# Kernel optimization log

Hardware: AMD Instinct MI355X
Metric: run time of the kernel (lower is better)

Reference implementation:

```python
import jax, jax.numpy as jnp
import numpy as np

BUCKET_SIZE = 64  # init kwarg bucket_size
DIM = 64          # init kwarg dim (per-head dim, used for scaling)


def setup_inputs() -> dict:
    key = jax.random.key(0)
    kq, kk = jax.random.split(key)
    q = jax.random.normal(kq, (32, 8192, 64), dtype=jnp.float32)
    k = jax.random.normal(kk, (32, 8192, 64), dtype=jnp.float32)
    return {"q": q, "k": k}


def _cumavg(t):
    # cumulative average along the sequence axis (axis=1)
    r = jnp.arange(1, t.shape[1] + 1, dtype=t.dtype)
    return jnp.cumsum(t, axis=1) / r[None, :, None]


def reference(q, k):
    bh, n, d = q.shape
    buckets = n // BUCKET_SIZE
    kv_buckets = k.shape[1] // BUCKET_SIZE

    # bucket the cumulative averages: [bh, buckets, bucket_size, d]
    q_r = _cumavg(q).reshape(bh, buckets, BUCKET_SIZE, d)
    k_r = _cumavg(k).reshape(bh, kv_buckets, BUCKET_SIZE, d)

    sq = q_r[:, :, 0]                                   # [bh, buckets, d]
    sk = k_r.sum(axis=2)                                # [bh, kv_buckets, d]
    sk = jnp.pad(sk, ((0, 0), (1, 0), (0, 0)))          # pad one zero bucket row at front

    R = jnp.einsum('bie,bje->bij', sq, sk) * (DIM ** -0.5)  # [bh, buckets, kv_buckets+1]

    rows = jnp.arange(buckets)[:, None]
    cols = jnp.arange(kv_buckets + 1)[None, :]
    neg = -jnp.finfo(R.dtype).max
    # masked_fill: for row i, columns i+1..buckets set to -max (cols > rows)
    R = jnp.where(cols > rows, neg, R)
    R = jax.nn.softmax(R, axis=-1)
    # tril(diagonal=-1): keep entries with col < row
    R = jnp.where(cols < rows, R, jnp.zeros((), R.dtype))
    return R
```

## Files before the change

kernel.cpp:

```cpp
#include <hip/hip_runtime.h>
#include <cstddef>
#include <cstdint>

constexpr int BH = 32;
constexpr int N  = 8192;
constexpr int D  = 64;
constexpr int BK = 64;
constexpr int NB = 128;
constexpr int NC = 129;

#define GLOBAL_AS(p) ((const __attribute__((address_space(1))) uint32_t*)(p))
#define LDS_AS(p)    ((__attribute__((address_space(3))) uint32_t*)(p))

__global__ __launch_bounds__(256) void kA(const float* __restrict__ q,
                                          const float* __restrict__ k,
                                          float* __restrict__ qsum,
                                          float* __restrict__ ksum,
                                          float* __restrict__ kw,
                                          float* __restrict__ qfirst,
                                          float* __restrict__ W) {
  const int j = blockIdx.x, b = blockIdx.y;
  const int tid  = threadIdx.x;
  const int f    = tid & 15;
  const int rr   = tid >> 4;
  const int w    = tid >> 6;
  const int lane = tid & 63;
  const int base = j * BK;
  const size_t ob = ((size_t)b * NB + j) * D;

  __shared__ float4 buf4[2048];
  __shared__ float red[3][4][D];

  const float4* q4 = (const float4*)(q + ((size_t)b * N + base) * D);
  const float4* k4 = (const float4*)(k + ((size_t)b * N + base) * D);

#pragma unroll
  for (int p = 0; p < 4; ++p) {
    const int u = w * 256 + p * 64 + lane;
    __builtin_amdgcn_global_load_lds(GLOBAL_AS(q4 + u), LDS_AS(buf4 + u), 16, 0, 0);
    __builtin_amdgcn_global_load_lds(GLOBAL_AS(k4 + u), LDS_AS(buf4 + 1024 + u), 16, 0, 0);
  }

  float x = 1.0f / (float)(base + lane + 1);
#pragma unroll
  for (int s = 1; s < 64; s <<= 1) {
    const float y = __shfl_down(x, s, 64);
    if (lane + s < 64) x += y;
  }
  float tw[4];
#pragma unroll
  for (int p = 0; p < 4; ++p) tw[p] = __shfl(x, 16 * p + rr, 64);

  __syncthreads();

  float aq[4] = {0, 0, 0, 0}, ak[4] = {0, 0, 0, 0}, aw[4] = {0, 0, 0, 0};
#pragma unroll
  for (int p = 0; p < 4; ++p) {
    const float4 vq = buf4[(16 * p + rr) * 16 + f];
    const float4 vk = buf4[1024 + (16 * p + rr) * 16 + f];
    aq[0] += vq.x; aq[1] += vq.y; aq[2] += vq.z; aq[3] += vq.w;
    ak[0] += vk.x; ak[1] += vk.y; ak[2] += vk.z; ak[3] += vk.w;
    aw[0] += vk.x * tw[p]; aw[1] += vk.y * tw[p];
    aw[2] += vk.z * tw[p]; aw[3] += vk.w * tw[p];
  }

#pragma unroll
  for (int c = 0; c < 4; ++c) {
    aq[c] += __shfl_xor(aq[c], 16, 64); aq[c] += __shfl_xor(aq[c], 32, 64);
    ak[c] += __shfl_xor(ak[c], 16, 64); ak[c] += __shfl_xor(ak[c], 32, 64);
    aw[c] += __shfl_xor(aw[c], 16, 64); aw[c] += __shfl_xor(aw[c], 32, 64);
  }
  if (lane < 16) {
    ((float4*)&red[0][w][0])[f] = make_float4(aq[0], aq[1], aq[2], aq[3]);
    ((float4*)&red[1][w][0])[f] = make_float4(ak[0], ak[1], ak[2], ak[3]);
    ((float4*)&red[2][w][0])[f] = make_float4(aw[0], aw[1], aw[2], aw[3]);
  }
  if (tid < 16) {
    ((float4*)(qfirst + ob))[tid] = buf4[tid];
  }
  if (tid == 0 && b == 0) W[j] = x;
  __syncthreads();

  if (tid < 192) {
    const int arr = tid >> 6, d = tid & 63;
    const float s = red[arr][0][d] + red[arr][1][d] + red[arr][2][d] + red[arr][3][d];
    float* dst = (arr == 0) ? qsum : (arr == 1) ? ksum : kw;
    dst[ob + d] = s;
  }
}

__global__ __launch_bounds__(256) void kB(const float* __restrict__ qsum,
                                          const float* __restrict__ ksum,
                                          const float* __restrict__ kw,
                                          const float* __restrict__ qfirst,
                                          const float* __restrict__ W,
                                          float* __restrict__ sq,
                                          float* __restrict__ skp) {
  const int side = blockIdx.x;
  const int b    = blockIdx.y;
  const int tid  = threadIdx.x;
  const int d    = tid & 63;
  const int jg   = tid >> 6;

  __shared__ float buf[NB * D];
  __shared__ float tot[4 * D];
  __shared__ float Wl[NB];

  const float* src = (side == 0 ? qsum : ksum) + (size_t)b * NB * D;
  {
    const float4* g4 = (const float4*)src;
    float4* l4 = (float4*)buf;
    for (int u = tid; u < NB * D / 4; u += 256) l4[u] = g4[u];
    if (side == 1 && tid < NB) Wl[tid] = W[tid];
  }
  __syncthreads();

  float t0 = 0.0f;
  for (int jj = 0; jj < 32; ++jj) t0 += buf[(jg * 32 + jj) * D + d];
  tot[jg * D + d] = t0;
  __syncthreads();

  float pre = 0.0f;
  for (int g = 0; g < jg; ++g) pre += tot[g * D + d];

  if (side == 0) {
    for (int jj = 0; jj < 32; ++jj) {
      const int j = jg * 32 + jj;
      const size_t o = ((size_t)b * NB + j) * D + d;
      sq[o] = (pre + qfirst[o]) / (float)(j * BK + 1);
      pre += buf[j * D + d];
    }
  } else {
    if (tid < D) skp[(size_t)b * NC * D + tid] = 0.0f;
    for (int jj = 0; jj < 32; ++jj) {
      const int j = jg * 32 + jj;
      const size_t o = ((size_t)b * NB + j) * D + d;
      skp[((size_t)b * NC + j + 1) * D + d] = pre * Wl[j] + kw[o];
      pre += buf[j * D + d];
    }
  }
}

__global__ __launch_bounds__(256) void kC(const float* __restrict__ sq,
                                          const float* __restrict__ skp,
                                          float* __restrict__ out) {
  const int tile = blockIdx.x, b = blockIdx.y;
  const int tid = threadIdx.x;
  const int jp = tid & 63, rep = tid >> 6;
  const int T0 = tile * 8;
  const int rows = T0 + 8;

  __shared__ float skpS[NB * D];
  __shared__ float sqs[8 * D];

  {
    const float4* g4 = (const float4*)(skp + (size_t)b * NC * D);
    for (int u = tid; u < rows * 16; u += 256) {
      const int row = u >> 4, f = u & 15;
      ((float4*)skpS)[row * 16 + ((f + row) & 15)] = g4[u];
    }
    if (tid < 128)
      ((float4*)sqs)[tid] = ((const float4*)(sq + ((size_t)b * NB + T0) * D))[tid];
  }
  __syncthreads();

  float acc0[2] = {0, 0}, acc1[2] = {0, 0};
  const float4* sk4 = (const float4*)skpS;
  const float4* sq4 = (const float4*)sqs;
#pragma unroll
  for (int d4 = 0; d4 < 16; ++d4) {
    const int slot = (d4 + jp) & 15;
    const float4 k0 = sk4[jp * 16 + slot];
    const float4 k1 = sk4[(jp + 64) * 16 + slot];
#pragma unroll
    for (int ii = 0; ii < 2; ++ii) {
      const float4 s = sq4[(rep * 2 + ii) * 16 + d4];
      acc0[ii] += s.x * k0.x + s.y * k0.y + s.z * k0.z + s.w * k0.w;
      acc1[ii] += s.x * k1.x + s.y * k1.y + s.z * k1.z + s.w * k1.w;
    }
  }

#pragma unroll
  for (int ii = 0; ii < 2; ++ii) {
    const int i = T0 + rep * 2 + ii;
    const int j0 = jp, j1 = jp + 64;
    const float v0 = acc0[ii] * 0.125f, v1 = acc1[ii] * 0.125f;
    const bool val0 = (j0 <= i), val1 = (j1 <= i);
    float m = fmaxf(val0 ? v0 : -3.402823466e38f, val1 ? v1 : -3.402823466e38f);
#pragma unroll
    for (int s = 1; s < 64; s <<= 1) m = fmaxf(m, __shfl_xor(m, s, 64));
    const float e0 = val0 ? __expf(v0 - m) : 0.0f;
    const float e1 = val1 ? __expf(v1 - m) : 0.0f;
    float ss = e0 + e1;
#pragma unroll
    for (int s = 1; s < 64; s <<= 1) ss += __shfl_xor(ss, s, 64);
    const float rden = 1.0f / ss;
    float* orow = out + ((size_t)b * NB + i) * NC;
    orow[j0] = (j0 < i) ? e0 * rden : 0.0f;
    orow[j1] = (j1 < i) ? e1 * rden : 0.0f;
    if (jp == 0) orow[128] = 0.0f;
  }
}

extern "C" void kernel_launch(void* const* d_in, const int* in_sizes, int n_in,
                              void* d_out, int out_size, void* d_ws, size_t ws_size,
                              hipStream_t stream) {
  const float* q = (const float*)d_in[0];
  const float* k = (const float*)d_in[1];
  float* out = (float*)d_out;

  float* ws     = (float*)d_ws;
  float* qsum   = ws;
  float* ksum   = qsum   + (size_t)BH * NB * D;
  float* kw     = ksum   + (size_t)BH * NB * D;
  float* qfirst = kw     + (size_t)BH * NB * D;
  float* sq     = qfirst + (size_t)BH * NB * D;
  float* skp    = sq     + (size_t)BH * NB * D;
  float* W      = skp    + (size_t)BH * NC * D;

  kA<<<dim3(NB, BH), 256, 0, stream>>>(q, k, qsum, ksum, kw, qfirst, W);
  kB<<<dim3(2, BH), 256, 0, stream>>>(qsum, ksum, kw, qfirst, W, sq, skp);
  kC<<<dim3(16, BH), 256, 0, stream>>>(sq, skp, out);
}
```

Baseline: 155.9 us.

## Split kA across q and k sides and load directly into registers

The bucket-reduction kernel kA now launches a third grid dimension so that q and k buckets are handled by separate blocks, doubling the block count and halving per-block work. Global loads go straight to registers with nontemporal hints instead of global_load_lds into a 32KB LDS buffer. The prefix weights are computed by one wave and shared through a small LDS array instead of shuffles. This aims to raise occupancy and memory-level parallelism for the bandwidth-bound read of q and k. In exchange it adds a side-dependent branch and a conditional barrier.

```diff
diff --git a/kernel.cpp b/kernel.cpp
--- a/kernel.cpp
+++ b/kernel.cpp
@@ -1,6 +1,5 @@
 #include <hip/hip_runtime.h>
 #include <cstddef>
-#include <cstdint>
 
 constexpr int BH = 32;
 constexpr int N  = 8192;
@@ -9,8 +8,7 @@
 constexpr int NB = 128;
 constexpr int NC = 129;
 
-#define GLOBAL_AS(p) ((const __attribute__((address_space(1))) uint32_t*)(p))
-#define LDS_AS(p)    ((__attribute__((address_space(3))) uint32_t*)(p))
+typedef float v4f __attribute__((ext_vector_type(4)));
 
 __global__ __launch_bounds__(256) void kA(const float* __restrict__ q,
                                           const float* __restrict__ k,
@@ -19,73 +17,75 @@
                                           float* __restrict__ kw,
                                           float* __restrict__ qfirst,
                                           float* __restrict__ W) {
-  const int j = blockIdx.x, b = blockIdx.y;
-  const int tid  = threadIdx.x;
-  const int f    = tid & 15;
-  const int rr   = tid >> 4;
-  const int w    = tid >> 6;
-  const int lane = tid & 63;
+  const int j = blockIdx.x, b = blockIdx.y, side = blockIdx.z;
+  const int tid = threadIdx.x;
+  const int f = tid & 15, r = tid >> 4, w = tid >> 6, lane = tid & 63;
   const int base = j * BK;
+
+  __shared__ float tailw[BK];
+  __shared__ float red[2][4][D];
+
+  const float* src = (side == 0 ? q : k) + ((size_t)b * N + base) * D;
+  const v4f* s4 = (const v4f*)src;
+
+  v4f v[4];
+#pragma unroll
+  for (int p = 0; p < 4; ++p) v[p] = __builtin_nontemporal_load(&s4[(r + 16 * p) * 16 + f]);
+
+  if (side == 1) {
+    if (w == 0) {
+      float x = 1.0f / (float)(base + lane + 1);
+#pragma unroll
+      for (int s = 1; s < 64; s <<= 1) {
+        float y = __shfl_down(x, s, 64);
+        if (lane + s < 64) x += y;
+      }
+      tailw[lane] = x;
+      if (lane == 0 && b == 0) W[j] = x;
+    }
+    __syncthreads();
+  }
+
+  float a0[4] = {0, 0, 0, 0}, a1[4] = {0, 0, 0, 0};
+  if (side == 0) {
+#pragma unroll
+    for (int p = 0; p < 4; ++p) {
+      a0[0] += v[p].x; a0[1] += v[p].y; a0[2] += v[p].z; a0[3] += v[p].w;
+    }
+  } else {
+#pragma unroll
+    for (int p = 0; p < 4; ++p) {
+      const float tw = tailw[r + 16 * p];
+      a0[0] += v[p].x; a0[1] += v[p].y; a0[2] += v[p].z; a0[3] += v[p].w;
+      a1[0] += v[p].x * tw; a1[1] += v[p].y * tw;
+      a1[2] += v[p].z * tw; a1[3] += v[p].w * tw;
+    }
+  }
+
+#pragma unroll
+  for (int c = 0; c < 4; ++c) {
+    a0[c] += __shfl_xor(a0[c], 16, 64); a0[c] += __shfl_xor(a0[c], 32, 64);
+    a1[c] += __shfl_xor(a1[c], 16, 64); a1[c] += __shfl_xor(a1[c], 32, 64);
+  }
+  if (lane < 16) {
+    ((float4*)&red[0][w][0])[f] = make_float4(a0[0], a0[1], a0[2], a0[3]);
+    ((float4*)&red[1][w][0])[f] = make_float4(a1[0], a1[1], a1[2], a1[3]);
+  }
+  __syncthreads();
+
   const size_t ob = ((size_t)b * NB + j) * D;
-
-  __shared__ float4 buf4[2048];
-  __shared__ float red[3][4][D];
-
-  const float4* q4 = (const float4*)(q + ((size_t)b * N + base) * D);
-  const float4* k4 = (const float4*)(k + ((size_t)b * N + base) * D);
-
-#pragma unroll
-  for (int p = 0; p < 4; ++p) {
-    const int u = w * 256 + p * 64 + lane;
-    __builtin_amdgcn_global_load_lds(GLOBAL_AS(q4 + u), LDS_AS(buf4 + u), 16, 0, 0);
-    __builtin_amdgcn_global_load_lds(GLOBAL_AS(k4 + u), LDS_AS(buf4 + 1024 + u), 16, 0, 0);
-  }
-
-  float x = 1.0f / (float)(base + lane + 1);
-#pragma unroll
-  for (int s = 1; s < 64; s <<= 1) {
-    const float y = __shfl_down(x, s, 64);
-    if (lane + s < 64) x += y;
-  }
-  float tw[4];
-#pragma unroll
-  for (int p = 0; p < 4; ++p) tw[p] = __shfl(x, 16 * p + rr, 64);
-
-  __syncthreads();
-
-  float aq[4] = {0, 0, 0, 0}, ak[4] = {0, 0, 0, 0}, aw[4] = {0, 0, 0, 0};
-#pragma unroll
-  for (int p = 0; p < 4; ++p) {
-    const float4 vq = buf4[(16 * p + rr) * 16 + f];
-    const float4 vk = buf4[1024 + (16 * p + rr) * 16 + f];
-    aq[0] += vq.x; aq[1] += vq.y; aq[2] += vq.z; aq[3] += vq.w;
-    ak[0] += vk.x; ak[1] += vk.y; ak[2] += vk.z; ak[3] += vk.w;
-    aw[0] += vk.x * tw[p]; aw[1] += vk.y * tw[p];
-    aw[2] += vk.z * tw[p]; aw[3] += vk.w * tw[p];
-  }
-
-#pragma unroll
-  for (int c = 0; c < 4; ++c) {
-    aq[c] += __shfl_xor(aq[c], 16, 64); aq[c] += __shfl_xor(aq[c], 32, 64);
-    ak[c] += __shfl_xor(ak[c], 16, 64); ak[c] += __shfl_xor(ak[c], 32, 64);
-    aw[c] += __shfl_xor(aw[c], 16, 64); aw[c] += __shfl_xor(aw[c], 32, 64);
-  }
-  if (lane < 16) {
-    ((float4*)&red[0][w][0])[f] = make_float4(aq[0], aq[1], aq[2], aq[3]);
-    ((float4*)&red[1][w][0])[f] = make_float4(ak[0], ak[1], ak[2], ak[3]);
-    ((float4*)&red[2][w][0])[f] = make_float4(aw[0], aw[1], aw[2], aw[3]);
-  }
-  if (tid < 16) {
-    ((float4*)(qfirst + ob))[tid] = buf4[tid];
-  }
-  if (tid == 0 && b == 0) W[j] = x;
-  __syncthreads();
-
-  if (tid < 192) {
-    const int arr = tid >> 6, d = tid & 63;
-    const float s = red[arr][0][d] + red[arr][1][d] + red[arr][2][d] + red[arr][3][d];
-    float* dst = (arr == 0) ? qsum : (arr == 1) ? ksum : kw;
-    dst[ob + d] = s;
+  if (tid < D) {
+    const float s0 = red[0][0][tid] + red[0][1][tid] + red[0][2][tid] + red[0][3][tid];
+    if (side == 0) {
+      qsum[ob + tid] = s0;
+    } else {
+      ksum[ob + tid] = s0;
+      kw[ob + tid] = red[1][0][tid] + red[1][1][tid] + red[1][2][tid] + red[1][3][tid];
+    }
+  }
+  if (side == 0 && r == 0) {
+    v4f qf = v[0];
+    ((float4*)(qfirst + ob))[f] = make_float4(qf.x, qf.y, qf.z, qf.w);
   }
 }
 
@@ -218,7 +218,7 @@
   float* skp    = sq     + (size_t)BH * NB * D;
   float* W      = skp    + (size_t)BH * NC * D;
 
-  kA<<<dim3(NB, BH), 256, 0, stream>>>(q, k, qsum, ksum, kw, qfirst, W);
+  kA<<<dim3(NB, BH, 2), 256, 0, stream>>>(q, k, qsum, ksum, kw, qfirst, W);
   kB<<<dim3(2, BH), 256, 0, stream>>>(qsum, ksum, kw, qfirst, W, sq, skp);
   kC<<<dim3(16, BH), 256, 0, stream>>>(sq, skp, out);
 }
```

Result: faster. 149.7 us (-4.0%).
